# Optimization experiments

Hardware: AMD Instinct MI355X
Metric: run time of the kernel (lower is better)

Reference implementation:

```python
import jax, jax.numpy as jnp
import numpy as np

B, S, I, H, O, F = 8192, 100, 15, 128, 2, 30  # batch, seq, input, hidden, out, future


def _lstm_cell(x, h, c, w_ih, w_hh, b):
    # PyTorch gate order: input, forget, cell(g), output
    gates = x @ w_ih.T + h @ w_hh.T + b  # [B, 4H]
    i, f, g, o = jnp.split(gates, 4, axis=-1)
    c2 = jax.nn.sigmoid(f) * c + jax.nn.sigmoid(i) * jnp.tanh(g)
    h2 = jax.nn.sigmoid(o) * jnp.tanh(c2)
    return h2, c2


def setup_inputs() -> dict:
    key = jax.random.key(0)
    ks = jax.random.split(key, 12)
    s = 1.0 / np.sqrt(H)  # PyTorch LSTM/Linear init scale
    u = lambda k, shape: jax.random.uniform(k, shape, jnp.float32, -s, s)
    return {
        "x": jax.random.normal(ks[0], (B, S, I), jnp.float32),
        "w_ih0": u(ks[1], (4 * H, I)),
        "w_hh0": u(ks[2], (4 * H, H)),
        "b_ih0": u(ks[3], (4 * H,)),
        "b_hh0": u(ks[4], (4 * H,)),
        "w_ih1": u(ks[5], (4 * H, H)),
        "w_hh1": u(ks[6], (4 * H, H)),
        "b_ih1": u(ks[7], (4 * H,)),
        "b_hh1": u(ks[8], (4 * H,)),
        "fc_w": u(ks[9], (O, H)),
        "fc_b": u(ks[10], (O,)),
        "future_frames": F,
    }


def reference(x, w_ih0, w_hh0, b_ih0, b_hh0, w_ih1, w_hh1, b_ih1, b_hh1, fc_w, fc_b, future_frames):
    bsz = x.shape[0]
    hid = w_hh0.shape[1]
    b0 = b_ih0 + b_hh0
    b1 = b_ih1 + b_hh1

    # ---- encoder: run full 2-layer LSTM over the observed sequence ----
    xs = jnp.transpose(x, (1, 0, 2))  # [S, B, I]
    z = jnp.zeros((bsz, hid), x.dtype)

    def enc_step(carry, xt):
        h0, c0, h1, c1 = carry
        h0, c0 = _lstm_cell(xt, h0, c0, w_ih0, w_hh0, b0)
        h1, c1 = _lstm_cell(h0, h1, c1, w_ih1, w_hh1, b1)
        return (h0, c0, h1, c1), None

    (h0, c0, h1, c1), _ = jax.lax.scan(enc_step, (z, z, z, z), xs)

    def dec_step(carry, _):
        h0, c0, h1, c1, inp = carry
        h0, c0 = _lstm_cell(inp, h0, c0, w_ih0, w_hh0, b0)
        h1, c1 = _lstm_cell(h0, h1, c1, w_ih1, w_hh1, b1)
        pred = h1 @ fc_w.T + fc_b  # [B, 2]
        nxt = inp.at[:, :2].set(pred)
        return (h0, c0, h1, c1, nxt), pred

    _, preds = jax.lax.scan(dec_step, (h0, c0, h1, c1, x[:, -1, :]), None, length=future_frames)
    return jnp.transpose(preds, (1, 0, 2))  # [B, future_frames, 2]
```

## Files before the change

kernel.cpp:

```cpp
#include <hip/hip_runtime.h>


typedef _Float16 half_t;
typedef _Float16 half8 __attribute__((ext_vector_type(8)));
typedef _Float16 half4 __attribute__((ext_vector_type(4)));
typedef float f32x4 __attribute__((ext_vector_type(4)));

#define SEQ 100
#define FUT 30
#define TOT (SEQ + FUT)
#define NIN 15
#define MB  32
#define CHK 25
#define L2E 1.44269504f
#define SH  136
#define SXS 20
#define SXX 16

#define MFMA32(A, B, C) __builtin_amdgcn_mfma_f32_16x16x32_f16((A), (B), (C), 0, 0, 0)
#define MFMA16(A, B, C) __builtin_amdgcn_mfma_f32_16x16x16f16((A), (B), (C), 0, 0, 0)

__global__ void prep_kernel(const float* __restrict__ w_ih0, const float* __restrict__ w_hh0,
                            const float* __restrict__ b_ih0, const float* __restrict__ b_hh0,
                            const float* __restrict__ w_ih1, const float* __restrict__ w_hh1,
                            const float* __restrict__ b_ih1, const float* __restrict__ b_hh1,
                            half_t* __restrict__ wsh)
{
  int idx = blockIdx.x * 256 + threadIdx.x;
  if (idx < 196608) {
    int seg = idx >> 16;
    int r   = idx & 65535;
    int n   = r >> 7, k = r & 127;
    int g   = (n >> 4) & 3;
    int row = g * 128 + ((n >> 6) << 4) + (n & 15);
    float sc = (g == 2) ? (2.0f * L2E) : (-L2E);
    const float* src = (seg == 0) ? w_hh0 : ((seg == 1) ? w_ih1 : w_hh1);
    wsh[idx] = (half_t)(src[row * 128 + k] * sc);
  } else if (idx < 204800) {
    int r   = idx - 196608;
    int n   = r >> 4, k = r & 15;
    int g   = (n >> 4) & 3;
    int row = g * 128 + ((n >> 6) << 4) + (n & 15);
    float sc = (g == 2) ? (2.0f * L2E) : (-L2E);
    float v;
    if (k < NIN) v = w_ih0[row * NIN + k] * sc;
    else         v = (b_ih0[row] + b_hh0[row]) * sc;
    wsh[idx] = (half_t)v;
  } else if (idx < 205824) {
    int r     = idx - 204800;
    float* bv = (float*)(wsh + 204800);
    int which = r >> 9, n = r & 511;
    int g     = (n >> 4) & 3;
    int row   = g * 128 + ((n >> 6) << 4) + (n & 15);
    float sc  = (g == 2) ? (2.0f * L2E) : (-L2E);
    bv[r] = ((which == 0) ? (b_ih0[row] + b_hh0[row]) : (b_ih1[row] + b_hh1[row])) * sc;
  }
}

__global__ __launch_bounds__(512, 2)
void lstm_kernel(const float* __restrict__ x,
                 const half_t* __restrict__ wsh,
                 const float* __restrict__ fcw,
                 const float* __restrict__ fcb,
                 float* __restrict__ out)
{
  __shared__ __align__(16) half_t sxc[CHK * MB * SXX];
  __shared__ __align__(16) half_t sh0[2][MB * SH];
  __shared__ __align__(16) half_t sh1[2][MB * SH];
  __shared__ __align__(16) half_t swx[512 * SXS];
  __shared__ __align__(16) half_t sdec[MB * SXX];
  __shared__ __align__(16) float  sbias[512];
  __shared__ __align__(16) float  sfc[258];
  __shared__ __align__(16) float  sc0[2][512 * 4];
  __shared__ __align__(16) float  sc1[2][512 * 4];

  const half_t* WH0 = wsh;
  const half_t* WI1 = wsh + 65536;
  const half_t* WH1 = wsh + 131072;
  const half_t* WX  = wsh + 196608;
  const float*  BV  = (const float*)(wsh + 204800);

  const int tid   = threadIdx.x;
  const int wave  = tid >> 6;
  const int lane  = tid & 63;
  const int l16   = lane & 15;
  const int quad  = lane >> 4;
  const int nb    = wave * 64;
  const int bbase = blockIdx.x * MB;
  const int wcol  = wave * 16 + l16;

  half8 wh0[4][4], wi1[4][4], wh1[4][4];
  #pragma unroll
  for (int kt = 0; kt < 4; ++kt) {
    #pragma unroll
    for (int g = 0; g < 4; ++g) {
      int n = nb + g * 16 + l16;
      int k = kt * 32 + quad * 8;
      wh0[kt][g] = *(const half8*)&WH0[n * 128 + k];
      wi1[kt][g] = *(const half8*)&WI1[n * 128 + k];
      wh1[kt][g] = *(const half8*)&WH1[n * 128 + k];
    }
  }

  for (int it = tid; it < 8192; it += 512) {
    int n = it >> 4, k = it & 15;
    swx[n * SXS + k] = WX[it];
  }
  for (int it = tid; it < 512; it += 512) sbias[it] = BV[512 + it];
  if (tid < 256) sfc[tid] = fcw[tid];
  if (tid < 2)   sfc[256 + tid] = fcb[tid];
  {
    int b = tid >> 4, i = tid & 15;
    sdec[b * SXX + i] = (i < NIN) ? (half_t)x[(size_t)(bbase + b) * (SEQ * NIN) + 99 * NIN + i]
                                  : (half_t)1.0f;
  }
  for (int it = tid; it < MB * SH; it += 512) {
    sh0[0][it] = (half_t)0; sh0[1][it] = (half_t)0;
    sh1[0][it] = (half_t)0; sh1[1][it] = (half_t)0;
  }
  {
    f32x4 z = (f32x4){0.f, 0.f, 0.f, 0.f};
    *(f32x4*)&sc0[0][tid * 4] = z; *(f32x4*)&sc0[1][tid * 4] = z;
    *(f32x4*)&sc1[0][tid * 4] = z; *(f32x4*)&sc1[1][tid * 4] = z;
  }
  __syncthreads();

  #define ACT_STORE(ACC, CV, DST, MT)                                          \
    _Pragma("unroll")                                                          \
    for (int r = 0; r < 4; ++r) {                                              \
      float A  = __builtin_amdgcn_exp2f((ACC)[0][r]);                          \
      float C  = __builtin_amdgcn_exp2f((ACC)[1][r]);                          \
      float B  = __builtin_amdgcn_exp2f((ACC)[2][r]);                          \
      float D  = __builtin_amdgcn_exp2f((ACC)[3][r]);                          \
      float oA = 1.f + A, oB = 1.f + B, oC = 1.f + C, oD = 1.f + D;            \
      float P  = oA * oB;                                                      \
      float t  = (B - 1.f) * oC;                                               \
      float nm = fmaf((CV)[r], P, t);                                          \
      float rc = __builtin_amdgcn_rcpf(P * oC);                                \
      float cn = nm * rc;                                                      \
      (CV)[r] = cn;                                                            \
      float E  = __builtin_amdgcn_exp2f(2.0f * L2E * cn);                      \
      float h  = (E - 1.f) * __builtin_amdgcn_rcpf(oD * (1.f + E));            \
      int   m  = (MT) * 16 + quad * 4 + r;                                     \
      (DST)[m * SH + wcol] = (half_t)h;                                        \
    }

  int cur = 0;
  for (int s = 0; s < TOT; ++s) {
    const int nxt = cur ^ 1;

    if (s < SEQ && (s % CHK) == 0) {
      for (int it = tid; it < MB * CHK * NIN; it += 512) {
        int b  = it / (CHK * NIN);
        int r2 = it - b * (CHK * NIN);
        int sc = r2 / NIN;
        int i  = r2 - sc * NIN;
        sxc[(sc * MB + b) * SXX + i] =
            (half_t)x[(size_t)(bbase + b) * (SEQ * NIN) + (s + sc) * NIN + i];
      }
      for (int it = tid; it < CHK * MB; it += 512) sxc[it * SXX + 15] = (half_t)1.0f;
      __syncthreads();
    }
    const half_t* xsrc = (s < SEQ) ? &sxc[(s % CHK) * MB * SXX] : sdec;

    #pragma unroll
    for (int mt = 0; mt < 2; ++mt) {
      f32x4 cv = *(const f32x4*)&sc0[mt][tid * 4];
      f32x4 acc[4];
      #pragma unroll
      for (int g = 0; g < 4; ++g) acc[g] = (f32x4){0.f, 0.f, 0.f, 0.f};
      #pragma unroll
      for (int kt = 0; kt < 4; ++kt) {
        int c = kt * 4 + quad;
        half8 ah = *(const half8*)&sh0[cur][(mt * 16 + l16) * SH + c * 8];
        #pragma unroll
        for (int g = 0; g < 4; ++g) acc[g] = MFMA32(ah, wh0[kt][g], acc[g]);
      }
      half4 ax = *(const half4*)&xsrc[(mt * 16 + l16) * SXX + quad * 4];
      #pragma unroll
      for (int g = 0; g < 4; ++g) {
        half4 bx = *(const half4*)&swx[(nb + g * 16 + l16) * SXS + quad * 4];
        acc[g] = MFMA16(ax, bx, acc[g]);
      }
      ACT_STORE(acc, cv, (&sh0[nxt][0]), mt)
      *(f32x4*)&sc0[mt][tid * 4] = cv;
    }
    __syncthreads();

    #pragma unroll
    for (int mt = 0; mt < 2; ++mt) {
      f32x4 cv = *(const f32x4*)&sc1[mt][tid * 4];
      f32x4 acc[4];
      #pragma unroll
      for (int g = 0; g < 4; ++g) {
        float b = sbias[nb + g * 16 + l16];
        acc[g] = (f32x4){b, b, b, b};
      }
      #pragma unroll
      for (int kt = 0; kt < 4; ++kt) {
        int c = kt * 4 + quad;
        half8 ah = *(const half8*)&sh0[nxt][(mt * 16 + l16) * SH + c * 8];
        #pragma unroll
        for (int g = 0; g < 4; ++g) acc[g] = MFMA32(ah, wi1[kt][g], acc[g]);
      }
      #pragma unroll
      for (int kt = 0; kt < 4; ++kt) {
        int c = kt * 4 + quad;
        half8 ah = *(const half8*)&sh1[cur][(mt * 16 + l16) * SH + c * 8];
        #pragma unroll
        for (int g = 0; g < 4; ++g) acc[g] = MFMA32(ah, wh1[kt][g], acc[g]);
      }
      ACT_STORE(acc, cv, (&sh1[nxt][0]), mt)
      *(f32x4*)&sc1[mt][tid * 4] = cv;
    }

    if (s >= SEQ) {
      __syncthreads();
      {
        int b   = wave * 4 + (lane >> 4);
        int o   = (lane >> 3) & 1;
        int seg = lane & 7;
        float p = 0.f;
        #pragma unroll
        for (int cc = 0; cc < 2; ++cc) {
          int c = seg * 2 + cc;
          half8 hv = *(const half8*)&sh1[nxt][b * SH + c * 8];
          f32x4 w0 = *(const f32x4*)&sfc[o * 128 + c * 8];
          f32x4 w1 = *(const f32x4*)&sfc[o * 128 + c * 8 + 4];
          #pragma unroll
          for (int u = 0; u < 4; ++u) p = fmaf((float)hv[u], w0[u], p);
          #pragma unroll
          for (int u = 0; u < 4; ++u) p = fmaf((float)hv[4 + u], w1[u], p);
        }
        p += __shfl_down(p, 4);
        p += __shfl_down(p, 2);
        p += __shfl_down(p, 1);
        if (seg == 0) {
          p += sfc[256 + o];
          out[(size_t)(bbase + b) * (FUT * 2) + (s - SEQ) * 2 + o] = p;
          sdec[b * SXX + o] = (half_t)p;
        }
      }
      __syncthreads();
    }

    cur = nxt;
  }
}

extern "C" void kernel_launch(void* const* d_in, const int* in_sizes, int n_in,
                              void* d_out, int out_size, void* d_ws, size_t ws_size,
                              hipStream_t stream)
{
  (void)in_sizes; (void)n_in; (void)out_size; (void)ws_size;
  const float* x     = (const float*)d_in[0];
  const float* w_ih0 = (const float*)d_in[1];
  const float* w_hh0 = (const float*)d_in[2];
  const float* b_ih0 = (const float*)d_in[3];
  const float* b_hh0 = (const float*)d_in[4];
  const float* w_ih1 = (const float*)d_in[5];
  const float* w_hh1 = (const float*)d_in[6];
  const float* b_ih1 = (const float*)d_in[7];
  const float* b_hh1 = (const float*)d_in[8];
  const float* fcw   = (const float*)d_in[9];
  const float* fcb   = (const float*)d_in[10];
  float*  out = (float*)d_out;
  half_t* wsh = (half_t*)d_ws;

  prep_kernel<<<(205824 + 255) / 256, 256, 0, stream>>>(
      w_ih0, w_hh0, b_ih0, b_hh0, w_ih1, w_hh1, b_ih1, b_hh1, wsh);
  lstm_kernel<<<8192 / MB, 512, 0, stream>>>(x, wsh, fcw, fcb, out);
}
```

Baseline: 592.0 us.

## Software-pipeline MFMA tiles with gate activations across LSTM layers and steps

Restructures each timestep so that the MFMAs for one 16-row batch tile are interleaved with the transcendental gate activations of the other tile. The recurrent h0 GEMM for the next step is also hoisted into the tail of the layer-1 phase, overlapping it with layer-1 activations. The aim is to hide MFMA latency behind VALU exp/rcp work instead of running them serially. The cost is higher register pressure from several live accumulator sets, plus a cross-iteration dependency on sh0[nxt] being ready before the next step's accumulation.

```diff
diff --git a/kernel.cpp b/kernel.cpp
--- a/kernel.cpp
+++ b/kernel.cpp
@@ -125,25 +125,36 @@
   }
   __syncthreads();
 
-  #define ACT_STORE(ACC, CV, DST, MT)                                          \
-    _Pragma("unroll")                                                          \
-    for (int r = 0; r < 4; ++r) {                                              \
-      float A  = __builtin_amdgcn_exp2f((ACC)[0][r]);                          \
-      float C  = __builtin_amdgcn_exp2f((ACC)[1][r]);                          \
-      float B  = __builtin_amdgcn_exp2f((ACC)[2][r]);                          \
-      float D  = __builtin_amdgcn_exp2f((ACC)[3][r]);                          \
+  #define ACT_ELEM(ACC, CV, DST, MT, R)                                        \
+    {                                                                          \
+      float A  = __builtin_amdgcn_exp2f((ACC)[0][R]);                          \
+      float C  = __builtin_amdgcn_exp2f((ACC)[1][R]);                          \
+      float B  = __builtin_amdgcn_exp2f((ACC)[2][R]);                          \
+      float D  = __builtin_amdgcn_exp2f((ACC)[3][R]);                          \
       float oA = 1.f + A, oB = 1.f + B, oC = 1.f + C, oD = 1.f + D;            \
       float P  = oA * oB;                                                      \
       float t  = (B - 1.f) * oC;                                               \
-      float nm = fmaf((CV)[r], P, t);                                          \
+      float nm = fmaf((CV)[R], P, t);                                          \
       float rc = __builtin_amdgcn_rcpf(P * oC);                                \
       float cn = nm * rc;                                                      \
-      (CV)[r] = cn;                                                            \
+      (CV)[R] = cn;                                                            \
       float E  = __builtin_amdgcn_exp2f(2.0f * L2E * cn);                      \
       float h  = (E - 1.f) * __builtin_amdgcn_rcpf(oD * (1.f + E));            \
-      int   m  = (MT) * 16 + quad * 4 + r;                                     \
+      int   m  = (MT) * 16 + quad * 4 + (R);                                   \
       (DST)[m * SH + wcol] = (half_t)h;                                        \
     }
+
+  f32x4 accP[4];
+
+  #pragma unroll
+  for (int g = 0; g < 4; ++g) accP[g] = (f32x4){0.f, 0.f, 0.f, 0.f};
+  #pragma unroll
+  for (int kt = 0; kt < 4; ++kt) {
+    int c = kt * 4 + quad;
+    half8 ah = *(const half8*)&sh0[0][l16 * SH + c * 8];
+    #pragma unroll
+    for (int g = 0; g < 4; ++g) accP[g] = MFMA32(ah, wh0[kt][g], accP[g]);
+  }
 
   int cur = 0;
   for (int s = 0; s < TOT; ++s) {
@@ -163,56 +174,95 @@
     }
     const half_t* xsrc = (s < SEQ) ? &sxc[(s % CHK) * MB * SXX] : sdec;
 
-    #pragma unroll
-    for (int mt = 0; mt < 2; ++mt) {
-      f32x4 cv = *(const f32x4*)&sc0[mt][tid * 4];
-      f32x4 acc[4];
-      #pragma unroll
-      for (int g = 0; g < 4; ++g) acc[g] = (f32x4){0.f, 0.f, 0.f, 0.f};
-      #pragma unroll
-      for (int kt = 0; kt < 4; ++kt) {
-        int c = kt * 4 + quad;
-        half8 ah = *(const half8*)&sh0[cur][(mt * 16 + l16) * SH + c * 8];
-        #pragma unroll
-        for (int g = 0; g < 4; ++g) acc[g] = MFMA32(ah, wh0[kt][g], acc[g]);
-      }
-      half4 ax = *(const half4*)&xsrc[(mt * 16 + l16) * SXX + quad * 4];
+    {
+      half4 ax = *(const half4*)&xsrc[l16 * SXX + quad * 4];
       #pragma unroll
       for (int g = 0; g < 4; ++g) {
         half4 bx = *(const half4*)&swx[(nb + g * 16 + l16) * SXS + quad * 4];
-        acc[g] = MFMA16(ax, bx, acc[g]);
+        accP[g] = MFMA16(ax, bx, accP[g]);
       }
-      ACT_STORE(acc, cv, (&sh0[nxt][0]), mt)
-      *(f32x4*)&sc0[mt][tid * 4] = cv;
-    }
+    }
+
+    f32x4 cv00 = *(const f32x4*)&sc0[0][tid * 4];
+    f32x4 cv01 = *(const f32x4*)&sc0[1][tid * 4];
+    f32x4 accQ[4];
+    #pragma unroll
+    for (int g = 0; g < 4; ++g) accQ[g] = (f32x4){0.f, 0.f, 0.f, 0.f};
+    #pragma unroll
+    for (int r = 0; r < 4; ++r) {
+      ACT_ELEM(accP, cv00, (&sh0[nxt][0]), 0, r)
+      int c = r * 4 + quad;
+      half8 ah = *(const half8*)&sh0[cur][(16 + l16) * SH + c * 8];
+      #pragma unroll
+      for (int g = 0; g < 4; ++g) accQ[g] = MFMA32(ah, wh0[r][g], accQ[g]);
+    }
+    *(f32x4*)&sc0[0][tid * 4] = cv00;
+    {
+      half4 ax = *(const half4*)&xsrc[(16 + l16) * SXX + quad * 4];
+      #pragma unroll
+      for (int g = 0; g < 4; ++g) {
+        half4 bx = *(const half4*)&swx[(nb + g * 16 + l16) * SXS + quad * 4];
+        accQ[g] = MFMA16(ax, bx, accQ[g]);
+      }
+    }
+    #pragma unroll
+    for (int r = 0; r < 4; ++r) ACT_ELEM(accQ, cv01, (&sh0[nxt][0]), 1, r)
+    *(f32x4*)&sc0[1][tid * 4] = cv01;
     __syncthreads();
 
-    #pragma unroll
-    for (int mt = 0; mt < 2; ++mt) {
-      f32x4 cv = *(const f32x4*)&sc1[mt][tid * 4];
-      f32x4 acc[4];
-      #pragma unroll
-      for (int g = 0; g < 4; ++g) {
-        float b = sbias[nb + g * 16 + l16];
-        acc[g] = (f32x4){b, b, b, b};
-      }
-      #pragma unroll
-      for (int kt = 0; kt < 4; ++kt) {
-        int c = kt * 4 + quad;
-        half8 ah = *(const half8*)&sh0[nxt][(mt * 16 + l16) * SH + c * 8];
-        #pragma unroll
-        for (int g = 0; g < 4; ++g) acc[g] = MFMA32(ah, wi1[kt][g], acc[g]);
-      }
-      #pragma unroll
-      for (int kt = 0; kt < 4; ++kt) {
-        int c = kt * 4 + quad;
-        half8 ah = *(const half8*)&sh1[cur][(mt * 16 + l16) * SH + c * 8];
-        #pragma unroll
-        for (int g = 0; g < 4; ++g) acc[g] = MFMA32(ah, wh1[kt][g], acc[g]);
-      }
-      ACT_STORE(acc, cv, (&sh1[nxt][0]), mt)
-      *(f32x4*)&sc1[mt][tid * 4] = cv;
-    }
+    f32x4 cv10 = *(const f32x4*)&sc1[0][tid * 4];
+    f32x4 cv11 = *(const f32x4*)&sc1[1][tid * 4];
+    f32x4 accR[4];
+    #pragma unroll
+    for (int g = 0; g < 4; ++g) {
+      float b = sbias[nb + g * 16 + l16];
+      accR[g] = (f32x4){b, b, b, b};
+    }
+    #pragma unroll
+    for (int kt = 0; kt < 4; ++kt) {
+      int c = kt * 4 + quad;
+      half8 ah = *(const half8*)&sh0[nxt][l16 * SH + c * 8];
+      #pragma unroll
+      for (int g = 0; g < 4; ++g) accR[g] = MFMA32(ah, wi1[kt][g], accR[g]);
+    }
+    #pragma unroll
+    for (int kt = 0; kt < 4; ++kt) {
+      int c = kt * 4 + quad;
+      half8 ah = *(const half8*)&sh1[cur][l16 * SH + c * 8];
+      #pragma unroll
+      for (int g = 0; g < 4; ++g) accR[g] = MFMA32(ah, wh1[kt][g], accR[g]);
+    }
+
+    f32x4 accS[4];
+    #pragma unroll
+    for (int g = 0; g < 4; ++g) {
+      float b = sbias[nb + g * 16 + l16];
+      accS[g] = (f32x4){b, b, b, b};
+    }
+    #pragma unroll
+    for (int r = 0; r < 4; ++r) {
+      ACT_ELEM(accR, cv10, (&sh1[nxt][0]), 0, r)
+      int c = r * 4 + quad;
+      half8 ah0 = *(const half8*)&sh0[nxt][(16 + l16) * SH + c * 8];
+      #pragma unroll
+      for (int g = 0; g < 4; ++g) accS[g] = MFMA32(ah0, wi1[r][g], accS[g]);
+      half8 ah1 = *(const half8*)&sh1[cur][(16 + l16) * SH + c * 8];
+      #pragma unroll
+      for (int g = 0; g < 4; ++g) accS[g] = MFMA32(ah1, wh1[r][g], accS[g]);
+    }
+    *(f32x4*)&sc1[0][tid * 4] = cv10;
+
+    #pragma unroll
+    for (int g = 0; g < 4; ++g) accP[g] = (f32x4){0.f, 0.f, 0.f, 0.f};
+    #pragma unroll
+    for (int r = 0; r < 4; ++r) {
+      ACT_ELEM(accS, cv11, (&sh1[nxt][0]), 1, r)
+      int c = r * 4 + quad;
+      half8 ah = *(const half8*)&sh0[nxt][l16 * SH + c * 8];
+      #pragma unroll
+      for (int g = 0; g < 4; ++g) accP[g] = MFMA32(ah, wh0[r][g], accP[g]);
+    }
+    *(f32x4*)&sc1[1][tid * 4] = cv11;
 
     if (s >= SEQ) {
       __syncthreads();
```

Result: slower. 2.008 ms (+239.3%).
